# Performance work log

Measured on AMD Instinct MI355X. Metric: run time of the kernel, lower is better.

## Reference

```python
import jax, jax.numpy as jnp
import numpy as np

B, U, C, M = 4096, 1024, 5000, 20

def setup_inputs() -> dict:
    key = jax.random.key(0)
    ks = jax.random.split(key, 9)
    inputs = jax.random.randint(ks[0], (B, 1), 0, C).astype(jnp.int32)
    states = 0.1 * jax.random.normal(ks[1], (B, U + 2), dtype=jnp.float32)
    bias_z = jnp.zeros((U,), jnp.float32)
    recurrent_kernel = 0.02 * jax.random.normal(ks[2], (U, 4 * U), dtype=jnp.float32)
    kernel_c = 0.02 * jax.random.normal(ks[3], (C, 4 * U), dtype=jnp.float32)
    bias = jnp.zeros((3 * U,), jnp.float32)
    kernel_d = 0.1 * jax.random.normal(ks[4], (2, 4 * U), dtype=jnp.float32)
    Wgmm_part1 = 0.05 * jax.random.normal(ks[5], (U, 3 * M), dtype=jnp.float32)
    bgmm_part1 = jnp.zeros((3 * M,), jnp.float32)
    return {"inputs": inputs, "states": states, "bias_z": bias_z,
            "recurrent_kernel": recurrent_kernel, "kernel_c": kernel_c,
            "bias": bias, "kernel_d": kernel_d,
            "Wgmm_part1": Wgmm_part1, "bgmm_part1": bgmm_part1}

def exp_safe(x):
    return jnp.clip(jnp.exp(x), 1e-10, 1e10)

def reference(inputs, states, bias_z, recurrent_kernel, kernel_c, bias,
              kernel_d, Wgmm_part1, bgmm_part1):
    u = bias_z.shape[0]
    h_tm1 = states[:, :-2]          # [B, U]
    _d = states[:, -2:]             # [B, 2]
    ch = inputs[:, 0].astype(jnp.int32)
    # one_hot(ch) @ kernel_c is just a row gather
    pre = kernel_c[ch] + _d @ kernel_d              # [B, 4U]
    # z and r gates share the left operand -> fuse into one matmul
    zr = (h_tm1 @ recurrent_kernel[:, :2 * u] + pre[:, :2 * u]
          + jnp.concatenate([bias_z, bias[:u]]))
    z = jax.nn.sigmoid(zr[:, :u])
    r = jax.nn.sigmoid(zr[:, u:])
    hh = jnp.tanh((r * h_tm1) @ recurrent_kernel[:, 2 * u:3 * u]
                  + pre[:, 2 * u:3 * u] + bias[u:2 * u])
    h = z * h_tm1 + (1.0 - z) * hh
    o = jnp.tanh(h @ recurrent_kernel[:, 3 * u:]
                 + pre[:, 3 * u:] + bias[2 * u:])
    gmm = o @ Wgmm_part1 + bgmm_part1               # [B, 3M]
    _pi, mux, muy = jnp.split(gmm, 3, axis=-1)
    e = exp_safe(_pi)
    pi = e / jnp.sum(e, axis=-1, keepdims=True)
    x_pred = jnp.sum(pi * mux, axis=-1, keepdims=True)
    y_pred = jnp.sum(pi * muy, axis=-1, keepdims=True)
    out = jnp.concatenate([o, pi, mux, muy, x_pred, y_pred], axis=-1)
    new_state = jnp.concatenate([h, x_pred, y_pred], axis=-1)
    return out, new_state
```

## Files before the change

### kernel.cpp

```cpp
#include <hip/hip_runtime.h>

typedef __attribute__((ext_vector_type(8))) short     bf16x8;
typedef __attribute__((ext_vector_type(4))) float     f32x4;
typedef __attribute__((ext_vector_type(2))) float     f32x2;
typedef __attribute__((ext_vector_type(4))) unsigned short u16x4;

#define OUT_STRIDE 1086
#define NS_STRIDE 1026
#define NS_BASE (4096*1086)

__device__ __forceinline__ unsigned short f2bf(float x) {
  unsigned int u = __float_as_uint(x);
  unsigned int r = (u + 0x7FFFu + ((u >> 16) & 1u)) >> 16;
  return (unsigned short)r;
}
__device__ __forceinline__ float bf2f(unsigned short u) {
  union { unsigned int i; float f; } v; v.i = ((unsigned int)u) << 16; return v.f;
}
__device__ __forceinline__ float sigmoidf(float x) { return 1.f / (1.f + expf(-x)); }

__device__ __forceinline__ void gld_lds16(const void* g, void* l) {
  __builtin_amdgcn_global_load_lds((const __attribute__((address_space(1))) void*)g,
                                   (__attribute__((address_space(3))) void*)l, 16, 0, 0);
}

__device__ __forceinline__ void decode_block(int bid, int& m0, int& n0) {
  const int swz = (bid & 7) * 64 + (bid >> 3);
  const int chunk = swz >> 6, l = swz & 63;
  m0 = ((chunk & 3) * 8 + (l >> 3)) * 128;
  n0 = ((chunk >> 2) * 8 + (l & 7)) * 64;
}

__global__ __launch_bounds__(256)
void transposeR(const float* __restrict__ R, unsigned short* __restrict__ Bt) {
  __shared__ float t[64][65];
  const int tx = threadIdx.x & 63, ty = threadIdx.x >> 6;
  const int j0 = blockIdx.x * 64, k0 = blockIdx.y * 64;
#pragma unroll
  for (int i = 0; i < 64; i += 4)
    t[ty + i][tx] = R[(size_t)(k0 + ty + i) * 4096 + j0 + tx];
  __syncthreads();
#pragma unroll
  for (int i = 0; i < 64; i += 4) {
    const int j = ty + i;
    Bt[(size_t)(j0 + j) * 1024 + k0 + tx] = f2bf(t[tx][j]);
  }
}

__global__ __launch_bounds__(256)
void convertH(const float* __restrict__ states, unsigned short* __restrict__ hb) {
  const int idx = blockIdx.x * 256 + threadIdx.x;
  const int b = idx >> 8, u = (idx & 255) * 4;
  const float* sp = states + (size_t)b * 1026 + u;
  f32x2 v0 = *(const f32x2*)sp, v1 = *(const f32x2*)(sp + 2);
  u16x4 w;
  w[0] = f2bf(v0[0]); w[1] = f2bf(v0[1]); w[2] = f2bf(v1[0]); w[3] = f2bf(v1[1]);
  *(u16x4*)&hb[(size_t)b * 1024 + u] = w;
}

__global__ __launch_bounds__(256)
void prep_wgt(const float* __restrict__ Wg, unsigned short* __restrict__ WgT) {
  const int idx = blockIdx.x * 256 + threadIdx.x;
  const int c = idx & 63, kq = idx >> 6;
#pragma unroll
  for (int j = 0; j < 4; ++j) {
    const int k = kq * 4 + j;
    WgT[(size_t)c * 1024 + k] = (c < 60) ? f2bf(Wg[(size_t)k * 60 + c]) : (unsigned short)0;
  }
}

__global__ __launch_bounds__(256)
void gemm_zr(const unsigned short* __restrict__ A,
             const unsigned short* __restrict__ Bt,
             const int* __restrict__ chv,
             const float* __restrict__ states,
             const float* __restrict__ kc,
             const float* __restrict__ kd,
             const float* __restrict__ bias_z,
             const float* __restrict__ bias,
             float* __restrict__ zbuf,
             unsigned short* __restrict__ rh) {
  __shared__ unsigned short Al[4][128 * 32];
  __shared__ unsigned short Bzl[4][64 * 32];
  __shared__ unsigned short Brl[4][64 * 32];
  __shared__ int   chs[128];
  __shared__ float d0s[128], d1s[128];

  const int tid = threadIdx.x, lane = tid & 63, wave = tid >> 6;
  int m0, n0;
  decode_block(blockIdx.x, m0, n0);

  if (tid < 128) {
    const int r = m0 + tid;
    chs[tid] = chv[r];
    d0s[tid] = states[(size_t)r * 1026 + 1024];
    d1s[tid] = states[(size_t)r * 1026 + 1025];
  }

  const unsigned short* Ag  = A  + (size_t)m0 * 1024;
  const unsigned short* Bzg = Bt + (size_t)n0 * 1024;
  const unsigned short* Brg = Bt + (size_t)(1024 + n0) * 1024;

  const int c1 = tid + 256;
  const int ar0 = tid >> 2, ak0 = (tid & 3) * 8;
  const int ar1 = c1 >> 2,  ak1 = (c1 & 3) * 8;

  f32x4 accz[2][4] = {}, accr[2][4] = {};
  const int arow = lane & 15, kg = (lane >> 4) * 8;

#define STAGE_ZR(b, kk)                                                        \
  gld_lds16(Ag  + (size_t)ar0 * 1024 + (kk) + ak0, &Al[b][tid * 8]);           \
  gld_lds16(Ag  + (size_t)ar1 * 1024 + (kk) + ak1, &Al[b][c1 * 8]);            \
  gld_lds16(Bzg + (size_t)ar0 * 1024 + (kk) + ak0, &Bzl[b][tid * 8]);          \
  gld_lds16(Brg + (size_t)ar0 * 1024 + (kk) + ak0, &Brl[b][tid * 8]);

  auto compute = [&](int cb) {
    bf16x8 af[2], bzf[4], brf[4];
#pragma unroll
    for (int mi = 0; mi < 2; ++mi)
      af[mi] = *(const bf16x8*)&Al[cb][(wave * 32 + mi * 16 + arow) * 32 + kg];
#pragma unroll
    for (int ni = 0; ni < 4; ++ni) {
      bzf[ni] = *(const bf16x8*)&Bzl[cb][(ni * 16 + arow) * 32 + kg];
      brf[ni] = *(const bf16x8*)&Brl[cb][(ni * 16 + arow) * 32 + kg];
    }
    __builtin_amdgcn_s_setprio(1);
#pragma unroll
    for (int mi = 0; mi < 2; ++mi)
#pragma unroll
      for (int ni = 0; ni < 4; ++ni) {
        accz[mi][ni] = __builtin_amdgcn_mfma_f32_16x16x32_bf16(af[mi], bzf[ni], accz[mi][ni], 0, 0, 0);
        accr[mi][ni] = __builtin_amdgcn_mfma_f32_16x16x32_bf16(af[mi], brf[ni], accr[mi][ni], 0, 0, 0);
      }
    __builtin_amdgcn_s_setprio(0);
  };

  STAGE_ZR(0, 0);
  STAGE_ZR(1, 32);
  for (int t = 0; t < 30; ++t) {
    const int nx = (t + 2) & 3;
    STAGE_ZR(nx, (t + 2) * 32);
    asm volatile("s_waitcnt vmcnt(8)" ::: "memory");
    __builtin_amdgcn_s_barrier();
    asm volatile("" ::: "memory");
    compute(t & 3);
  }
  asm volatile("s_waitcnt vmcnt(4)" ::: "memory");
  __builtin_amdgcn_s_barrier();
  asm volatile("" ::: "memory");
  compute(2);
  asm volatile("s_waitcnt vmcnt(0)" ::: "memory");
  __builtin_amdgcn_s_barrier();
  asm volatile("" ::: "memory");
  compute(3);
#undef STAGE_ZR

#pragma unroll
  for (int mi = 0; mi < 2; ++mi) {
#pragma unroll
    for (int r = 0; r < 4; ++r) {
      const int lrow = wave * 32 + mi * 16 + (lane >> 4) * 4 + r;
      const int grow = m0 + lrow;
      const int ch = chs[lrow];
      const float d0 = d0s[lrow], d1 = d1s[lrow];
      const float* kcrow = kc + (size_t)ch * 4096;
#pragma unroll
      for (int ni = 0; ni < 4; ++ni) {
        const int jc = n0 + ni * 16 + (lane & 15);
        const float vz = accz[mi][ni][r] + kcrow[jc]
                       + d0 * kd[jc] + d1 * kd[4096 + jc] + bias_z[jc];
        const float vr = accr[mi][ni][r] + kcrow[1024 + jc]
                       + d0 * kd[1024 + jc] + d1 * kd[4096 + 1024 + jc] + bias[jc];
        const float z = sigmoidf(vz);
        const float rr = sigmoidf(vr);
        zbuf[(size_t)grow * 1024 + jc] = z;
        rh[(size_t)grow * 1024 + jc] = f2bf(rr * bf2f(A[(size_t)grow * 1024 + jc]));
      }
    }
  }
}

template<int EPI>
__global__ __launch_bounds__(256)
void gemm_k(const unsigned short* __restrict__ A,
            const unsigned short* __restrict__ Bt,
            const int* __restrict__ chv,
            const float* __restrict__ states,
            const float* __restrict__ kc, int colbase,
            const float* __restrict__ kd,
            const float* __restrict__ bias, int biasoff,
            const float* __restrict__ zbuf,
            float* __restrict__ out2,
            unsigned short* __restrict__ hb2) {
  __shared__ unsigned short Al[4][128 * 32];
  __shared__ unsigned short Bl[4][64 * 32];
  __shared__ int   chs[128];
  __shared__ float d0s[128], d1s[128];

  const int tid = threadIdx.x, lane = tid & 63, wave = tid >> 6;
  int m0, n0;
  decode_block(blockIdx.x, m0, n0);

  if (tid < 128) {
    const int r = m0 + tid;
    chs[tid] = chv[r];
    d0s[tid] = states[(size_t)r * 1026 + 1024];
    d1s[tid] = states[(size_t)r * 1026 + 1025];
  }

  const unsigned short* Ag = A  + (size_t)m0 * 1024;
  const unsigned short* Bg = Bt + (size_t)n0 * 1024;

  const int c1 = tid + 256;
  const int ar0 = tid >> 2, ak0 = (tid & 3) * 8;
  const int ar1 = c1 >> 2,  ak1 = (c1 & 3) * 8;

  f32x4 acc[2][4] = {};
  const int arow = lane & 15, kg = (lane >> 4) * 8;

#define STAGE_K(b, kk)                                                         \
  gld_lds16(Ag + (size_t)ar0 * 1024 + (kk) + ak0, &Al[b][tid * 8]);            \
  gld_lds16(Ag + (size_t)ar1 * 1024 + (kk) + ak1, &Al[b][c1 * 8]);             \
  gld_lds16(Bg + (size_t)ar0 * 1024 + (kk) + ak0, &Bl[b][tid * 8]);

  auto compute = [&](int cb) {
    bf16x8 af[2], bfr[4];
#pragma unroll
    for (int mi = 0; mi < 2; ++mi)
      af[mi] = *(const bf16x8*)&Al[cb][(wave * 32 + mi * 16 + arow) * 32 + kg];
#pragma unroll
    for (int ni = 0; ni < 4; ++ni)
      bfr[ni] = *(const bf16x8*)&Bl[cb][(ni * 16 + arow) * 32 + kg];
    __builtin_amdgcn_s_setprio(1);
#pragma unroll
    for (int mi = 0; mi < 2; ++mi)
#pragma unroll
      for (int ni = 0; ni < 4; ++ni)
        acc[mi][ni] = __builtin_amdgcn_mfma_f32_16x16x32_bf16(af[mi], bfr[ni], acc[mi][ni], 0, 0, 0);
    __builtin_amdgcn_s_setprio(0);
  };

  STAGE_K(0, 0);
  STAGE_K(1, 32);
  for (int t = 0; t < 30; ++t) {
    const int nx = (t + 2) & 3;
    STAGE_K(nx, (t + 2) * 32);
    asm volatile("s_waitcnt vmcnt(6)" ::: "memory");
    __builtin_amdgcn_s_barrier();
    asm volatile("" ::: "memory");
    compute(t & 3);
  }
  asm volatile("s_waitcnt vmcnt(3)" ::: "memory");
  __builtin_amdgcn_s_barrier();
  asm volatile("" ::: "memory");
  compute(2);
  asm volatile("s_waitcnt vmcnt(0)" ::: "memory");
  __builtin_amdgcn_s_barrier();
  asm volatile("" ::: "memory");
  compute(3);
#undef STAGE_K

#pragma unroll
  for (int mi = 0; mi < 2; ++mi) {
#pragma unroll
    for (int r = 0; r < 4; ++r) {
      const int lrow = wave * 32 + mi * 16 + (lane >> 4) * 4 + r;
      const int grow = m0 + lrow;
      const int ch = chs[lrow];
      const float d0 = d0s[lrow], d1 = d1s[lrow];
      const float* kcrow = kc + (size_t)ch * 4096 + colbase;
#pragma unroll
      for (int ni = 0; ni < 4; ++ni) {
        const int gcol = n0 + ni * 16 + (lane & 15);
        float v = acc[mi][ni][r] + kcrow[gcol]
                + d0 * kd[colbase + gcol] + d1 * kd[4096 + colbase + gcol]
                + bias[biasoff + gcol];
        if (EPI == 2) {
          const float hh = tanhf(v);
          const float z = zbuf[(size_t)grow * 1024 + gcol];
          const float htm = states[(size_t)grow * 1026 + gcol];
          const float h = z * htm + (1.f - z) * hh;
          out2[(size_t)grow * NS_STRIDE + gcol] = h;
          hb2[(size_t)grow * 1024 + gcol] = f2bf(h);
        } else {
          const float o = tanhf(v);
          out2[(size_t)grow * OUT_STRIDE + gcol] = o;
          hb2[(size_t)grow * 1024 + gcol] = f2bf(o);
        }
      }
    }
  }
}

__global__ __launch_bounds__(256)
void gmm2(const unsigned short* __restrict__ ob,
          const unsigned short* __restrict__ WgT,
          const float* __restrict__ bg,
          float* __restrict__ outp,
          float* __restrict__ ns) {
  __shared__ float red[3 * 16 * 64];
  const int tid = threadIdx.x, lane = tid & 63, wave = tid >> 6;
  const int arow = lane & 15, q = lane >> 4;
  const int r0 = blockIdx.x * 16;

  const unsigned short* Al = ob  + (size_t)(r0 + arow) * 1024 + q * 8 + wave * 256;
  const unsigned short* Bl = WgT + (size_t)arow * 1024 + q * 8 + wave * 256;

  f32x4 acc[4] = {};
#pragma unroll
  for (int t = 0; t < 8; ++t) {
    const bf16x8 af = *(const bf16x8*)(Al + t * 32);
#pragma unroll
    for (int ni = 0; ni < 4; ++ni) {
      const bf16x8 bf_ = *(const bf16x8*)(Bl + (size_t)ni * 16 * 1024 + t * 32);
      acc[ni] = __builtin_amdgcn_mfma_f32_16x16x32_bf16(af, bf_, acc[ni], 0, 0, 0);
    }
  }

  if (wave) {
#pragma unroll
    for (int ni = 0; ni < 4; ++ni)
#pragma unroll
      for (int i = 0; i < 4; ++i)
        red[(wave - 1) * 1024 + (ni * 4 + i) * 64 + lane] = acc[ni][i];
  }
  __syncthreads();
  if (wave == 0) {
#pragma unroll
    for (int w = 0; w < 3; ++w)
#pragma unroll
      for (int ni = 0; ni < 4; ++ni)
#pragma unroll
        for (int i = 0; i < 4; ++i)
          acc[ni][i] += red[w * 1024 + (ni * 4 + i) * 64 + lane];

    const int gb = lane & 48;
#pragma unroll
    for (int i = 0; i < 4; ++i) {
      float g0 = acc[0][i] + bg[arow];
      float g1 = acc[1][i] + ((16 + arow < 60) ? bg[16 + arow] : 0.f);
      float g2 = acc[2][i] + ((32 + arow < 60) ? bg[32 + arow] : 0.f);
      float g3 = acc[3][i] + ((48 + arow < 60) ? bg[48 + arow] : 0.f);

      const float e0 = fminf(fmaxf(expf(g0), 1e-10f), 1e10f);
      const float e1 = (arow < 4) ? fminf(fmaxf(expf(g1), 1e-10f), 1e10f) : 0.f;
      float s = e0 + e1;
#pragma unroll
      for (int m = 1; m < 16; m <<= 1) s += __shfl_xor(s, m, 64);
      const float pi0 = e0 / s;
      const float pi1 = e1 / s;

      const float t1 = __shfl(g1, gb | ((arow + 4) & 15), 64);
      const float t2 = __shfl(g2, gb | ((arow + 4) & 15), 64);
      const float muxA = (arow < 12) ? t1 : t2;
      const float muxB = t2;
      const float u1 = __shfl(g2, gb | ((arow + 8) & 15), 64);
      const float u2 = __shfl(g3, gb | ((arow + 8) & 15), 64);
      const float muyA = (arow < 8) ? u1 : u2;
      const float muyB = u2;

      float px = pi0 * muxA + ((arow < 4) ? pi1 * muxB : 0.f);
      float py = pi0 * muyA + ((arow < 4) ? pi1 * muyB : 0.f);
#pragma unroll
      for (int m = 1; m < 16; m <<= 1) {
        px += __shfl_xor(px, m, 64);
        py += __shfl_xor(py, m, 64);
      }

      const int row = r0 + q * 4 + i;
      float* orow = outp + (size_t)row * OUT_STRIDE;
      orow[1024 + arow] = pi0;
      if (arow < 4)  orow[1040 + arow] = pi1;
      if (arow >= 4) orow[1040 + arow] = g1;
      orow[1056 + arow] = g2;
      if (arow < 12) orow[1072 + arow] = g3;
      if (arow == 0) {
        orow[1084] = px;
        orow[1085] = py;
        ns[(size_t)row * NS_STRIDE + 1024] = px;
        ns[(size_t)row * NS_STRIDE + 1025] = py;
      }
    }
  }
}

extern "C" void kernel_launch(void* const* d_in, const int* in_sizes, int n_in,
                              void* d_out, int out_size, void* d_ws, size_t ws_size,
                              hipStream_t stream) {
  const int*   chv    = (const int*)d_in[0];
  const float* states = (const float*)d_in[1];
  const float* bias_z = (const float*)d_in[2];
  const float* R      = (const float*)d_in[3];
  const float* kc     = (const float*)d_in[4];
  const float* bias   = (const float*)d_in[5];
  const float* kd     = (const float*)d_in[6];
  const float* Wg     = (const float*)d_in[7];
  const float* bg     = (const float*)d_in[8];
  float* out = (float*)d_out;

  char* ws = (char*)d_ws;
  unsigned short* RbT  = (unsigned short*)ws;
  unsigned short* hb   = (unsigned short*)(ws + 8388608);
  unsigned short* rh   = (unsigned short*)(ws + 16777216);
  unsigned short* hb2  = (unsigned short*)(ws + 25165824);
  float*          zbuf = (float*)(ws + 33554432);
  unsigned short* WgT  = (unsigned short*)(ws + 50331648);

  transposeR<<<dim3(64, 16), 256, 0, stream>>>(R, RbT);
  convertH<<<4096, 256, 0, stream>>>(states, hb);
  prep_wgt<<<64, 256, 0, stream>>>(Wg, WgT);

  gemm_zr<<<512, 256, 0, stream>>>(hb, RbT, chv, states, kc, kd, bias_z, bias, zbuf, rh);

  gemm_k<2><<<512, 256, 0, stream>>>(rh, RbT + (size_t)2048 * 1024,
      chv, states, kc, 2048, kd, bias, 1024, zbuf, out + NS_BASE, hb2);

  gemm_k<3><<<512, 256, 0, stream>>>(hb2, RbT + (size_t)3072 * 1024,
      chv, states, kc, 3072, kd, bias, 2048, nullptr, out, hb);

  gmm2<<<256, 256, 0, stream>>>(hb, WgT, bg, out, out + NS_BASE);
}
```

Baseline: 310.2 us.

## Switch GEMMs to single-wave 64x64 tiles with swizzled LDS and deeper prefetch

Replaces the 256-thread 128x64-tile GEMM kernels with 64-thread single-wavefront kernels, each computing a 64x64 tile (4x4 MFMA fragments per wave). Dropping block barriers and XOR-swizzling the LDS layout is meant to remove barrier stalls and LDS bank conflicts, and a 3-stage-ahead prefetch with tuned vmcnt waits is meant to hide global latency. In exchange each block holds more accumulators per thread, gets less A/B reuse per block, and the grid doubles to 1024 blocks.

```diff
diff --git a/kernel.cpp b/kernel.cpp
--- a/kernel.cpp
+++ b/kernel.cpp
@@ -23,13 +23,14 @@
   __builtin_amdgcn_global_load_lds((const __attribute__((address_space(1))) void*)g,
                                    (__attribute__((address_space(3))) void*)l, 16, 0, 0);
 }
-
-__device__ __forceinline__ void decode_block(int bid, int& m0, int& n0) {
-  const int swz = (bid & 7) * 64 + (bid >> 3);
-  const int chunk = swz >> 6, l = swz & 63;
-  m0 = ((chunk & 3) * 8 + (l >> 3)) * 128;
-  n0 = ((chunk >> 2) * 8 + (l & 7)) * 64;
-}
+#define MFMA(a, b, c) __builtin_amdgcn_mfma_f32_16x16x32_bf16(a, b, c, 0, 0, 0)
+
+#define VMW(n) { if ((n) == 36) asm volatile("s_waitcnt vmcnt(36)" ::: "memory");    \
+                 else if ((n) == 24) asm volatile("s_waitcnt vmcnt(24)" ::: "memory");\
+                 else if ((n) == 16) asm volatile("s_waitcnt vmcnt(16)" ::: "memory");\
+                 else if ((n) == 12) asm volatile("s_waitcnt vmcnt(12)" ::: "memory");\
+                 else if ((n) == 8)  asm volatile("s_waitcnt vmcnt(8)"  ::: "memory");\
+                 else asm volatile("s_waitcnt vmcnt(0)" ::: "memory"); }
 
 __global__ __launch_bounds__(256)
 void transposeR(const float* __restrict__ R, unsigned short* __restrict__ Bt) {
@@ -69,107 +70,84 @@
   }
 }
 
-__global__ __launch_bounds__(256)
-void gemm_zr(const unsigned short* __restrict__ A,
-             const unsigned short* __restrict__ Bt,
-             const int* __restrict__ chv,
-             const float* __restrict__ states,
-             const float* __restrict__ kc,
-             const float* __restrict__ kd,
-             const float* __restrict__ bias_z,
-             const float* __restrict__ bias,
-             float* __restrict__ zbuf,
-             unsigned short* __restrict__ rh) {
-  __shared__ unsigned short Al[4][128 * 32];
-  __shared__ unsigned short Bzl[4][64 * 32];
-  __shared__ unsigned short Brl[4][64 * 32];
-  __shared__ int   chs[128];
-  __shared__ float d0s[128], d1s[128];
-
-  const int tid = threadIdx.x, lane = tid & 63, wave = tid >> 6;
-  int m0, n0;
-  decode_block(blockIdx.x, m0, n0);
-
-  if (tid < 128) {
-    const int r = m0 + tid;
-    chs[tid] = chv[r];
-    d0s[tid] = states[(size_t)r * 1026 + 1024];
-    d1s[tid] = states[(size_t)r * 1026 + 1025];
-  }
-
-  const unsigned short* Ag  = A  + (size_t)m0 * 1024;
-  const unsigned short* Bzg = Bt + (size_t)n0 * 1024;
-  const unsigned short* Brg = Bt + (size_t)(1024 + n0) * 1024;
-
-  const int c1 = tid + 256;
-  const int ar0 = tid >> 2, ak0 = (tid & 3) * 8;
-  const int ar1 = c1 >> 2,  ak1 = (c1 & 3) * 8;
-
-  f32x4 accz[2][4] = {}, accr[2][4] = {};
-  const int arow = lane & 15, kg = (lane >> 4) * 8;
-
-#define STAGE_ZR(b, kk)                                                        \
-  gld_lds16(Ag  + (size_t)ar0 * 1024 + (kk) + ak0, &Al[b][tid * 8]);           \
-  gld_lds16(Ag  + (size_t)ar1 * 1024 + (kk) + ak1, &Al[b][c1 * 8]);            \
-  gld_lds16(Bzg + (size_t)ar0 * 1024 + (kk) + ak0, &Bzl[b][tid * 8]);          \
-  gld_lds16(Brg + (size_t)ar0 * 1024 + (kk) + ak0, &Brl[b][tid * 8]);
-
-  auto compute = [&](int cb) {
-    bf16x8 af[2], bzf[4], brf[4];
-#pragma unroll
-    for (int mi = 0; mi < 2; ++mi)
-      af[mi] = *(const bf16x8*)&Al[cb][(wave * 32 + mi * 16 + arow) * 32 + kg];
+__global__ __launch_bounds__(64)
+void gemm1w(const unsigned short* __restrict__ A,
+            const unsigned short* __restrict__ Bt,
+            const int* __restrict__ chv,
+            const float* __restrict__ states,
+            const float* __restrict__ kcm,
+            const float* __restrict__ kd,
+            const float* __restrict__ bias_z,
+            const float* __restrict__ bias,
+            float* __restrict__ zbuf,
+            unsigned short* __restrict__ rh) {
+  __shared__ __align__(16) char lds[4][12288];
+  __shared__ int chs[64];
+  __shared__ float d0s[64], d1s[64];
+
+  const int l = threadIdx.x, bid = blockIdx.x;
+  const int mt = (bid & 7) * 8 + ((bid >> 3) & 7);
+  const int nt = bid >> 6;
+  const int m0 = mt * 64, n0 = nt * 64;
+
+  chs[l] = chv[m0 + l];
+  d0s[l] = states[(size_t)(m0 + l) * 1026 + 1024];
+  d1s[l] = states[(size_t)(m0 + l) * 1026 + 1025];
+
+  const int srow = l >> 2;
+  const int scol = ((l & 3) ^ ((l >> 3) & 3)) * 8;
+  const unsigned short* As  = A  + (size_t)(m0 + srow) * 1024 + scol;
+  const unsigned short* Bzs = Bt + (size_t)(n0 + srow) * 1024 + scol;
+  const unsigned short* Brs = Bt + (size_t)(1024 + n0 + srow) * 1024 + scol;
+
+#define ST1W(rg, k0) { _Pragma("unroll")                                          \
+    for (int j = 0; j < 4; ++j) {                                                 \
+      gld_lds16(As  + (size_t)j * 16384 + (k0), &lds[rg][j * 1024 + l * 16]);     \
+      gld_lds16(Bzs + (size_t)j * 16384 + (k0), &lds[rg][4096 + j * 1024 + l * 16]); \
+      gld_lds16(Brs + (size_t)j * 16384 + (k0), &lds[rg][8192 + j * 1024 + l * 16]); } }
+
+  const int arow = l & 15, q = l >> 4;
+  const int rdo = (q ^ ((arow >> 1) & 3)) * 16;
+  f32x4 accz[4][4] = {}, accr[4][4] = {};
+
+  ST1W(0, 0) ST1W(1, 32) ST1W(2, 64)
+
+#pragma unroll
+  for (int t = 0; t < 32; ++t) {
+    if (t < 29) ST1W((t + 3) & 3, (t + 3) * 32)
+    VMW(t < 29 ? 36 : (t == 29 ? 24 : (t == 30 ? 12 : 0)))
+    const char* Lb = lds[t & 3];
+    bf16x8 af[4];
+#pragma unroll
+    for (int mi = 0; mi < 4; ++mi)
+      af[mi] = *(const bf16x8*)(Lb + (mi * 16 + arow) * 64 + rdo);
 #pragma unroll
     for (int ni = 0; ni < 4; ++ni) {
-      bzf[ni] = *(const bf16x8*)&Bzl[cb][(ni * 16 + arow) * 32 + kg];
-      brf[ni] = *(const bf16x8*)&Brl[cb][(ni * 16 + arow) * 32 + kg];
-    }
-    __builtin_amdgcn_s_setprio(1);
-#pragma unroll
-    for (int mi = 0; mi < 2; ++mi)
-#pragma unroll
-      for (int ni = 0; ni < 4; ++ni) {
-        accz[mi][ni] = __builtin_amdgcn_mfma_f32_16x16x32_bf16(af[mi], bzf[ni], accz[mi][ni], 0, 0, 0);
-        accr[mi][ni] = __builtin_amdgcn_mfma_f32_16x16x32_bf16(af[mi], brf[ni], accr[mi][ni], 0, 0, 0);
-      }
-    __builtin_amdgcn_s_setprio(0);
-  };
-
-  STAGE_ZR(0, 0);
-  STAGE_ZR(1, 32);
-  for (int t = 0; t < 30; ++t) {
-    const int nx = (t + 2) & 3;
-    STAGE_ZR(nx, (t + 2) * 32);
-    asm volatile("s_waitcnt vmcnt(8)" ::: "memory");
-    __builtin_amdgcn_s_barrier();
-    asm volatile("" ::: "memory");
-    compute(t & 3);
-  }
-  asm volatile("s_waitcnt vmcnt(4)" ::: "memory");
-  __builtin_amdgcn_s_barrier();
-  asm volatile("" ::: "memory");
-  compute(2);
-  asm volatile("s_waitcnt vmcnt(0)" ::: "memory");
-  __builtin_amdgcn_s_barrier();
-  asm volatile("" ::: "memory");
-  compute(3);
-#undef STAGE_ZR
-
-#pragma unroll
-  for (int mi = 0; mi < 2; ++mi) {
-#pragma unroll
-    for (int r = 0; r < 4; ++r) {
-      const int lrow = wave * 32 + mi * 16 + (lane >> 4) * 4 + r;
+      const bf16x8 bz = *(const bf16x8*)(Lb + 4096 + (ni * 16 + arow) * 64 + rdo);
+#pragma unroll
+      for (int mi = 0; mi < 4; ++mi) accz[mi][ni] = MFMA(af[mi], bz, accz[mi][ni]);
+      const bf16x8 br = *(const bf16x8*)(Lb + 8192 + (ni * 16 + arow) * 64 + rdo);
+#pragma unroll
+      for (int mi = 0; mi < 4; ++mi) accr[mi][ni] = MFMA(af[mi], br, accr[mi][ni]);
+    }
+  }
+#undef ST1W
+
+#pragma unroll
+  for (int mi = 0; mi < 4; ++mi) {
+#pragma unroll
+    for (int i = 0; i < 4; ++i) {
+      const int lrow = mi * 16 + q * 4 + i;
       const int grow = m0 + lrow;
       const int ch = chs[lrow];
       const float d0 = d0s[lrow], d1 = d1s[lrow];
-      const float* kcrow = kc + (size_t)ch * 4096;
+      const float* kcr = kcm + (size_t)ch * 4096;
 #pragma unroll
       for (int ni = 0; ni < 4; ++ni) {
-        const int jc = n0 + ni * 16 + (lane & 15);
-        const float vz = accz[mi][ni][r] + kcrow[jc]
+        const int jc = n0 + ni * 16 + arow;
+        const float vz = accz[mi][ni][i] + kcr[jc]
                        + d0 * kd[jc] + d1 * kd[4096 + jc] + bias_z[jc];
-        const float vr = accr[mi][ni][r] + kcrow[1024 + jc]
+        const float vr = accr[mi][ni][i] + kcr[1024 + jc]
                        + d0 * kd[1024 + jc] + d1 * kd[4096 + 1024 + jc] + bias[jc];
         const float z = sigmoidf(vz);
         const float rr = sigmoidf(vr);
@@ -181,111 +159,90 @@
 }
 
 template<int EPI>
-__global__ __launch_bounds__(256)
-void gemm_k(const unsigned short* __restrict__ A,
-            const unsigned short* __restrict__ Bt,
-            const int* __restrict__ chv,
-            const float* __restrict__ states,
-            const float* __restrict__ kc, int colbase,
-            const float* __restrict__ kd,
-            const float* __restrict__ bias, int biasoff,
-            const float* __restrict__ zbuf,
-            float* __restrict__ out2,
-            unsigned short* __restrict__ hb2) {
-  __shared__ unsigned short Al[4][128 * 32];
-  __shared__ unsigned short Bl[4][64 * 32];
-  __shared__ int   chs[128];
-  __shared__ float d0s[128], d1s[128];
-
-  const int tid = threadIdx.x, lane = tid & 63, wave = tid >> 6;
-  int m0, n0;
-  decode_block(blockIdx.x, m0, n0);
-
-  if (tid < 128) {
-    const int r = m0 + tid;
-    chs[tid] = chv[r];
-    d0s[tid] = states[(size_t)r * 1026 + 1024];
-    d1s[tid] = states[(size_t)r * 1026 + 1025];
-  }
-
-  const unsigned short* Ag = A  + (size_t)m0 * 1024;
-  const unsigned short* Bg = Bt + (size_t)n0 * 1024;
-
-  const int c1 = tid + 256;
-  const int ar0 = tid >> 2, ak0 = (tid & 3) * 8;
-  const int ar1 = c1 >> 2,  ak1 = (c1 & 3) * 8;
-
-  f32x4 acc[2][4] = {};
-  const int arow = lane & 15, kg = (lane >> 4) * 8;
-
-#define STAGE_K(b, kk)                                                         \
-  gld_lds16(Ag + (size_t)ar0 * 1024 + (kk) + ak0, &Al[b][tid * 8]);            \
-  gld_lds16(Ag + (size_t)ar1 * 1024 + (kk) + ak1, &Al[b][c1 * 8]);             \
-  gld_lds16(Bg + (size_t)ar0 * 1024 + (kk) + ak0, &Bl[b][tid * 8]);
-
-  auto compute = [&](int cb) {
-    bf16x8 af[2], bfr[4];
-#pragma unroll
-    for (int mi = 0; mi < 2; ++mi)
-      af[mi] = *(const bf16x8*)&Al[cb][(wave * 32 + mi * 16 + arow) * 32 + kg];
-#pragma unroll
-    for (int ni = 0; ni < 4; ++ni)
-      bfr[ni] = *(const bf16x8*)&Bl[cb][(ni * 16 + arow) * 32 + kg];
-    __builtin_amdgcn_s_setprio(1);
-#pragma unroll
-    for (int mi = 0; mi < 2; ++mi)
-#pragma unroll
-      for (int ni = 0; ni < 4; ++ni)
-        acc[mi][ni] = __builtin_amdgcn_mfma_f32_16x16x32_bf16(af[mi], bfr[ni], acc[mi][ni], 0, 0, 0);
-    __builtin_amdgcn_s_setprio(0);
-  };
-
-  STAGE_K(0, 0);
-  STAGE_K(1, 32);
-  for (int t = 0; t < 30; ++t) {
-    const int nx = (t + 2) & 3;
-    STAGE_K(nx, (t + 2) * 32);
-    asm volatile("s_waitcnt vmcnt(6)" ::: "memory");
-    __builtin_amdgcn_s_barrier();
-    asm volatile("" ::: "memory");
-    compute(t & 3);
-  }
-  asm volatile("s_waitcnt vmcnt(3)" ::: "memory");
-  __builtin_amdgcn_s_barrier();
-  asm volatile("" ::: "memory");
-  compute(2);
-  asm volatile("s_waitcnt vmcnt(0)" ::: "memory");
-  __builtin_amdgcn_s_barrier();
-  asm volatile("" ::: "memory");
-  compute(3);
-#undef STAGE_K
-
-#pragma unroll
-  for (int mi = 0; mi < 2; ++mi) {
-#pragma unroll
-    for (int r = 0; r < 4; ++r) {
-      const int lrow = wave * 32 + mi * 16 + (lane >> 4) * 4 + r;
+__global__ __launch_bounds__(64)
+void gemmw(const unsigned short* __restrict__ A,
+           const unsigned short* __restrict__ Bt,
+           const int* __restrict__ chv,
+           const float* __restrict__ states,
+           const float* __restrict__ kcm, int colbase,
+           const float* __restrict__ kd,
+           const float* __restrict__ bias, int biasoff,
+           const float* __restrict__ zbuf,
+           float* __restrict__ outp,
+           unsigned short* __restrict__ hb2) {
+  __shared__ __align__(16) char lds[4][8192];
+  __shared__ int chs[64];
+  __shared__ float d0s[64], d1s[64];
+
+  const int l = threadIdx.x, bid = blockIdx.x;
+  const int mt = (bid & 7) * 8 + ((bid >> 3) & 7);
+  const int nt = bid >> 6;
+  const int m0 = mt * 64, n0 = nt * 64;
+
+  chs[l] = chv[m0 + l];
+  d0s[l] = states[(size_t)(m0 + l) * 1026 + 1024];
+  d1s[l] = states[(size_t)(m0 + l) * 1026 + 1025];
+
+  const int srow = l >> 2;
+  const int scol = ((l & 3) ^ ((l >> 3) & 3)) * 8;
+  const unsigned short* As = A  + (size_t)(m0 + srow) * 1024 + scol;
+  const unsigned short* Bs = Bt + (size_t)(n0 + srow) * 1024 + scol;
+
+#define STW(rg, k0) { _Pragma("unroll")                                           \
+    for (int j = 0; j < 4; ++j) {                                                 \
+      gld_lds16(As + (size_t)j * 16384 + (k0), &lds[rg][j * 1024 + l * 16]);      \
+      gld_lds16(Bs + (size_t)j * 16384 + (k0), &lds[rg][4096 + j * 1024 + l * 16]); } }
+
+  const int arow = l & 15, q = l >> 4;
+  const int rdo = (q ^ ((arow >> 1) & 3)) * 16;
+  f32x4 acc[4][4] = {};
+
+  STW(0, 0) STW(1, 32) STW(2, 64)
+
+#pragma unroll
+  for (int t = 0; t < 32; ++t) {
+    if (t < 29) STW((t + 3) & 3, (t + 3) * 32)
+    VMW(t < 29 ? 24 : (t == 29 ? 16 : (t == 30 ? 8 : 0)))
+    const char* Lb = lds[t & 3];
+    bf16x8 af[4];
+#pragma unroll
+    for (int mi = 0; mi < 4; ++mi)
+      af[mi] = *(const bf16x8*)(Lb + (mi * 16 + arow) * 64 + rdo);
+#pragma unroll
+    for (int ni = 0; ni < 4; ++ni) {
+      const bf16x8 bf_ = *(const bf16x8*)(Lb + 4096 + (ni * 16 + arow) * 64 + rdo);
+#pragma unroll
+      for (int mi = 0; mi < 4; ++mi) acc[mi][ni] = MFMA(af[mi], bf_, acc[mi][ni]);
+    }
+  }
+#undef STW
+
+#pragma unroll
+  for (int mi = 0; mi < 4; ++mi) {
+#pragma unroll
+    for (int i = 0; i < 4; ++i) {
+      const int lrow = mi * 16 + q * 4 + i;
       const int grow = m0 + lrow;
       const int ch = chs[lrow];
       const float d0 = d0s[lrow], d1 = d1s[lrow];
-      const float* kcrow = kc + (size_t)ch * 4096 + colbase;
+      const float* kcr = kcm + (size_t)ch * 4096 + colbase;
 #pragma unroll
       for (int ni = 0; ni < 4; ++ni) {
-        const int gcol = n0 + ni * 16 + (lane & 15);
-        float v = acc[mi][ni][r] + kcrow[gcol]
-                + d0 * kd[colbase + gcol] + d1 * kd[4096 + colbase + gcol]
-                + bias[biasoff + gcol];
+        const int gc = n0 + ni * 16 + arow;
+        const float v = acc[mi][ni][i] + kcr[gc]
+                      + d0 * kd[colbase + gc] + d1 * kd[4096 + colbase + gc]
+                      + bias[biasoff + gc];
         if (EPI == 2) {
           const float hh = tanhf(v);
-          const float z = zbuf[(size_t)grow * 1024 + gcol];
-          const float htm = states[(size_t)grow * 1026 + gcol];
+          const float z = zbuf[(size_t)grow * 1024 + gc];
+          const float htm = states[(size_t)grow * 1026 + gc];
           const float h = z * htm + (1.f - z) * hh;
-          out2[(size_t)grow * NS_STRIDE + gcol] = h;
-          hb2[(size_t)grow * 1024 + gcol] = f2bf(h);
+          outp[(size_t)grow * NS_STRIDE + gc] = h;
+          hb2[(size_t)grow * 1024 + gc] = f2bf(h);
         } else {
           const float o = tanhf(v);
-          out2[(size_t)grow * OUT_STRIDE + gcol] = o;
-          hb2[(size_t)grow * 1024 + gcol] = f2bf(o);
+          outp[(size_t)grow * OUT_STRIDE + gc] = o;
+          hb2[(size_t)grow * 1024 + gc] = f2bf(o);
         }
       }
     }
@@ -313,7 +270,7 @@
 #pragma unroll
     for (int ni = 0; ni < 4; ++ni) {
       const bf16x8 bf_ = *(const bf16x8*)(Bl + (size_t)ni * 16 * 1024 + t * 32);
-      acc[ni] = __builtin_amdgcn_mfma_f32_16x16x32_bf16(af, bf_, acc[ni], 0, 0, 0);
+      acc[ni] = MFMA(af, bf_, acc[ni]);
     }
   }
 
@@ -410,12 +367,12 @@
   convertH<<<4096, 256, 0, stream>>>(states, hb);
   prep_wgt<<<64, 256, 0, stream>>>(Wg, WgT);
 
-  gemm_zr<<<512, 256, 0, stream>>>(hb, RbT, chv, states, kc, kd, bias_z, bias, zbuf, rh);
-
-  gemm_k<2><<<512, 256, 0, stream>>>(rh, RbT + (size_t)2048 * 1024,
+  gemm1w<<<1024, 64, 0, stream>>>(hb, RbT, chv, states, kc, kd, bias_z, bias, zbuf, rh);
+
+  gemmw<2><<<1024, 64, 0, stream>>>(rh, RbT + (size_t)2048 * 1024,
       chv, states, kc, 2048, kd, bias, 1024, zbuf, out + NS_BASE, hb2);
 
-  gemm_k<3><<<512, 256, 0, stream>>>(hb2, RbT + (size_t)3072 * 1024,
+  gemmw<3><<<1024, 64, 0, stream>>>(hb2, RbT + (size_t)3072 * 1024,
       chv, states, kc, 3072, kd, bias, 2048, nullptr, out, hb);
 
   gmm2<<<256, 256, 0, stream>>>(hb, WgT, bg, out, out + NS_BASE);
```

Result: slower. 420.1 us (+35.4%).
